# Kernel tuning notes

Hardware: AMD Instinct MI355X
Metric: run time of the kernel (lower is better)

Reference implementation:

```python
import jax, jax.numpy as jnp
import numpy as np

jax.config.update("jax_enable_x64", True)

NNZ = 8_388_608        # number of sparse (feature_id, value) pairs
N_FEATURES = 8_192     # number of calibrated feature ids
N_BIN = 63             # bin boundaries per feature -> 64 bins
OUT_BITS = 22          # output id space = 1 << 22
GOLDEN32 = np.uint32(0x9E3779B9)  # Knuth multiplicative-hashing constant


def setup_inputs() -> dict:
    key = jax.random.key(0)
    k1, k2, k3 = jax.random.split(key, 3)
    input_keys = jax.random.randint(k1, (NNZ,), 0, 2 * N_FEATURES, dtype=jnp.int64)
    input_vals = jax.random.normal(k2, (NNZ,), dtype=jnp.float32)
    # Calibrated feature ids (sorted) and per-feature sorted bin boundaries.
    feature_ids = jnp.arange(N_FEATURES, dtype=jnp.int64)
    bin_vals = jnp.sort(
        jax.random.normal(k3, (N_FEATURES, N_BIN), dtype=jnp.float32), axis=1
    ).reshape(-1)
    return {
        "input_keys": input_keys,
        "input_vals": input_vals,
        "feature_ids": feature_ids,
        "bin_vals": bin_vals,
    }


def _lower_bound_bins(bin_vals_flat, feat_idx, vals, n_bin):
    """Per-value branchless binary search: bin = sum(bin_row < val).

    bin_vals_flat: [F * n_bin] row-sorted boundaries, feat_idx: [nnz] int,
    vals: [nnz] float. Returns [nnz] int32 bin index in [0, n_bin].
    """
    steps = int(np.ceil(np.log2(n_bin + 1)))  # 6 for n_bin=63
    base = feat_idx.astype(jnp.int64) * n_bin
    lo = jnp.zeros(vals.shape, dtype=jnp.int32)
    hi = jnp.full(vals.shape, n_bin, dtype=jnp.int32)
    for _ in range(steps):
        mid = (lo + hi) >> 1                       # in [0, n_bin]
        mid_safe = jnp.minimum(mid, n_bin - 1)     # gather-safe
        bv = bin_vals_flat[base + mid_safe]
        valid = lo < hi
        go_right = valid & (bv < vals)             # strict '<' => lower bound
        lo = jnp.where(go_right, mid + 1, lo)
        hi = jnp.where(valid & ~go_right, mid, hi)
    return lo


def reference(input_keys, input_vals, feature_ids, bin_vals):
    F = feature_ids.shape[0]
    n_bin = bin_vals.shape[0] // F
    mask = jnp.int64((1 << OUT_BITS) - 1)

    # --- find each key in the (sorted) calibrated feature-id table ---
    idx = jnp.searchsorted(feature_ids, input_keys)          # [nnz]
    idx_safe = jnp.minimum(idx, F - 1)
    calibrated = feature_ids[idx_safe] == input_keys          # [nnz] bool

    # --- bin assignment: bin = sum(bin_vals_row < val) ---
    bins = _lower_bound_bins(bin_vals, idx_safe, input_vals, n_bin)

    # --- 32-bit integer multiplicative hash of (feature_id, bin) ---
    h = (input_keys.astype(jnp.uint32) * GOLDEN32 + bins.astype(jnp.uint32)) * GOLDEN32
    hashed_key = h.astype(jnp.int64) & mask

    out_keys = jnp.where(calibrated, hashed_key, input_keys & mask)
    out_vals = jnp.where(calibrated, jnp.ones_like(input_vals), input_vals)
    # dense_shape of the resulting SparseTensor is [batch, 1 << OUT_BITS]
    return out_keys, out_vals
```

## Files before the change

### kernel.cpp

```cpp
#include <hip/hip_runtime.h>
#include <stdint.h>
#include <math.h>


#define GOLDEN   0x9E3779B9u
#define OUT_MASK ((1u << 22) - 1u)
#define NBIN  63
#define NPIV  8192
#define NKEY  16384
#define MAGIC 0xC0FFEE42u

typedef float fx4 __attribute__((ext_vector_type(4)));
typedef int   ix4 __attribute__((ext_vector_type(4)));
typedef unsigned ux4 __attribute__((ext_vector_type(4)));

__global__ __launch_bounds__(256) void build_tables_kernel(
    const int* __restrict__ fids, const float* __restrict__ bins,
    float* __restrict__ qtab, ux4* __restrict__ spiv_g,
    unsigned char* __restrict__ scal_g, int F)
{
    const int t = blockIdx.x * blockDim.x + threadIdx.x;
    if (t >= F * 64) return;
    const int r = t >> 6;
    const int j = t & 63;
    const int k = fids[r];
    const unsigned uk = (unsigned)k;
    const float* src = bins + (size_t)r * NBIN;

    if (uk < (unsigned)NPIV) {
        qtab[((size_t)uk << 6) + j] = (j < NBIN) ? src[j] : INFINITY;
        if (j == 0) {
            ux4 p;
            p.x = __float_as_uint(src[15]);
            p.y = __float_as_uint(src[31]);
            p.z = __float_as_uint(src[47]);
            p.w = uk ^ MAGIC;
            spiv_g[uk] = p;
        }
    } else if (uk < (unsigned)NKEY && j == 0) {
        scal_g[uk - NPIV] = (unsigned char)(0x40u | (uk & 63u));
    }
}

__device__ __forceinline__ void hd_fallback(
    int k, float v, const int* __restrict__ fids, const float* __restrict__ bins,
    int F, int fsteps, float& okey, float& oval)
{
    int lo = 0, hi = F;
    for (int s = 0; s < fsteps; ++s) {
        int  mid  = (lo + hi) >> 1;
        int  mids = min(mid, F - 1);
        int  fv   = fids[mids];
        bool valid = lo < hi;
        bool right = valid && (fv < k);
        lo = right ? mid + 1 : lo;
        hi = (valid && !right) ? mid : hi;
    }
    const int  idx_safe   = min(lo, F - 1);
    const bool calibrated = (fids[idx_safe] == k);
    const float* brow = bins + (size_t)idx_safe * NBIN;
    int blo = 0, bhi = NBIN;
    #pragma unroll
    for (int s = 0; s < 6; ++s) {
        int   mid  = (blo + bhi) >> 1;
        int   mids = min(mid, NBIN - 1);
        float bv   = brow[mids];
        bool  valid = blo < bhi;
        bool  right = valid && (bv < v);
        blo = right ? mid + 1 : blo;
        bhi = (valid && !right) ? mid : bhi;
    }
    const uint32_t h = ((uint32_t)k * GOLDEN + (uint32_t)blo) * GOLDEN;
    okey = calibrated ? (float)(h & OUT_MASK) : (float)((uint32_t)k & OUT_MASK);
    oval = calibrated ? 1.0f : v;
}

__device__ __forceinline__ int hd_cmp8(fx4 a, fx4 b, float v) {
    return (a.x < v) + (a.y < v) + (a.z < v) + (a.w < v)
         + (b.x < v) + (b.y < v) + (b.z < v) + (b.w < v);
}

__global__ __launch_bounds__(1024, 4) void hd_main_kernel(
    const int* __restrict__ keys, const float* __restrict__ vals,
    const int* __restrict__ fids, const float* __restrict__ bins,
    const float* __restrict__ qtab, const ux4* __restrict__ spiv_g,
    const unsigned char* __restrict__ scal_g,
    float* __restrict__ out_keys, float* __restrict__ out_vals,
    int n, int F, int fsteps, int nchunks)
{
    extern __shared__ char smem[];
    ux4*      spiv = reinterpret_cast<ux4*>(smem);
    unsigned* scal = reinterpret_cast<unsigned*>(smem + (size_t)NPIV * 16);

    const int tid = threadIdx.x;
    for (int i = tid; i < NPIV; i += (int)blockDim.x) spiv[i] = spiv_g[i];
    const unsigned* scal_g32 = reinterpret_cast<const unsigned*>(scal_g);
    for (int i = tid; i < NPIV / 4; i += (int)blockDim.x) scal[i] = scal_g32[i];
    __syncthreads();

    const unsigned char* scal_b = reinterpret_cast<const unsigned char*>(scal);
    const char* qb = reinterpret_cast<const char*>(qtab);
    const int nthreads = (int)(gridDim.x * blockDim.x);

    for (int c = blockIdx.x * blockDim.x + tid; c < nchunks; c += nthreads) {
        const int i0 = c * 4;
        int   k0, k1, k2, k3;
        float v0, v1, v2, v3;
        const bool full = (i0 + 3 < n);
        if (full) {
            const ix4 ka = __builtin_nontemporal_load(reinterpret_cast<const ix4*>(keys + i0));
            const fx4 va = __builtin_nontemporal_load(reinterpret_cast<const fx4*>(vals + i0));
            k0 = ka.x; k1 = ka.y; k2 = ka.z; k3 = ka.w;
            v0 = va.x; v1 = va.y; v2 = va.z; v3 = va.w;
        } else {
            k0 = keys[min(i0 + 0, n - 1)]; v0 = vals[min(i0 + 0, n - 1)];
            k1 = keys[min(i0 + 1, n - 1)]; v1 = vals[min(i0 + 1, n - 1)];
            k2 = keys[min(i0 + 2, n - 1)]; v2 = vals[min(i0 + 2, n - 1)];
            k3 = keys[min(i0 + 3, n - 1)]; v3 = vals[min(i0 + 3, n - 1)];
        }

        const unsigned u0 = (unsigned)k0, u1 = (unsigned)k1,
                       u2 = (unsigned)k2, u3 = (unsigned)k3;
        const ux4 h0 = spiv[u0 < (unsigned)NPIV ? u0 : 0u];
        const ux4 h1 = spiv[u1 < (unsigned)NPIV ? u1 : 0u];
        const ux4 h2 = spiv[u2 < (unsigned)NPIV ? u2 : 0u];
        const ux4 h3 = spiv[u3 < (unsigned)NPIV ? u3 : 0u];

#define HD_P2(J)                                                              \
        const bool cal##J = (u##J < (unsigned)NPIV) &&                        \
                            (h##J.w == (u##J ^ MAGIC));                       \
        const int  q##J = (__uint_as_float(h##J.x) < v##J)                    \
                        + (__uint_as_float(h##J.y) < v##J)                    \
                        + (__uint_as_float(h##J.z) < v##J);                   \
        const unsigned off##J = cal##J ? ((u##J << 8) + (unsigned)(q##J << 6))\
                                       : 0u;                                  \
        int qc##J = q##J << 4;                                                \
        const unsigned hs##J = u##J - (unsigned)NPIV;                         \
        const bool rare##J =                                                  \
            (u##J >= (unsigned)NKEY) ||                                       \
            ((hs##J < (unsigned)NPIV) &&                                      \
             (scal_b[hs##J < (unsigned)NPIV ? hs##J : 0u] ==                  \
              (unsigned char)(0x40u | (u##J & 63u))));
        HD_P2(0) HD_P2(1) HD_P2(2) HD_P2(3)
#undef HD_P2

        fx4 a0 = *reinterpret_cast<const fx4*>(qb + off0);
        fx4 b0 = *reinterpret_cast<const fx4*>(qb + off0 + 16);
        fx4 a1 = *reinterpret_cast<const fx4*>(qb + off1);
        fx4 b1 = *reinterpret_cast<const fx4*>(qb + off1 + 16);
        fx4 a2 = *reinterpret_cast<const fx4*>(qb + off2);
        fx4 b2 = *reinterpret_cast<const fx4*>(qb + off2 + 16);
        fx4 a3 = *reinterpret_cast<const fx4*>(qb + off3);
        fx4 b3 = *reinterpret_cast<const fx4*>(qb + off3 + 16);

        qc0 += hd_cmp8(a0, b0, v0);
        qc1 += hd_cmp8(a1, b1, v1);
        qc2 += hd_cmp8(a2, b2, v2);
        qc3 += hd_cmp8(a3, b3, v3);

        a0 = *reinterpret_cast<const fx4*>(qb + off0 + 32);
        b0 = *reinterpret_cast<const fx4*>(qb + off0 + 48);
        a1 = *reinterpret_cast<const fx4*>(qb + off1 + 32);
        b1 = *reinterpret_cast<const fx4*>(qb + off1 + 48);
        a2 = *reinterpret_cast<const fx4*>(qb + off2 + 32);
        b2 = *reinterpret_cast<const fx4*>(qb + off2 + 48);
        a3 = *reinterpret_cast<const fx4*>(qb + off3 + 32);
        b3 = *reinterpret_cast<const fx4*>(qb + off3 + 48);

        float ok0, ok1, ok2, ok3, ov0, ov1, ov2, ov3;
#define HD_P6(J)                                                              \
        {                                                                     \
            const int cnt = qc##J + hd_cmp8(a##J, b##J, v##J);                \
            const uint32_t h = (u##J * GOLDEN + (uint32_t)cnt) * GOLDEN;      \
            ok##J = cal##J ? (float)(h & OUT_MASK) : (float)(u##J & OUT_MASK);\
            ov##J = cal##J ? 1.0f : v##J;                                     \
        }
        HD_P6(0) HD_P6(1) HD_P6(2) HD_P6(3)
#undef HD_P6

        if (__builtin_expect(rare0 | rare1 | rare2 | rare3, 0)) {
            if (rare0) hd_fallback(k0, v0, fids, bins, F, fsteps, ok0, ov0);
            if (rare1) hd_fallback(k1, v1, fids, bins, F, fsteps, ok1, ov1);
            if (rare2) hd_fallback(k2, v2, fids, bins, F, fsteps, ok2, ov2);
            if (rare3) hd_fallback(k3, v3, fids, bins, F, fsteps, ok3, ov3);
        }

        if (full) {
            fx4 s;
            s.x = ok0; s.y = ok1; s.z = ok2; s.w = ok3;
            __builtin_nontemporal_store(s, reinterpret_cast<fx4*>(out_keys + i0));
            s.x = ov0; s.y = ov1; s.z = ov2; s.w = ov3;
            __builtin_nontemporal_store(s, reinterpret_cast<fx4*>(out_vals + i0));
        } else {
            if (i0 + 0 < n) { out_keys[i0 + 0] = ok0; out_vals[i0 + 0] = ov0; }
            if (i0 + 1 < n) { out_keys[i0 + 1] = ok1; out_vals[i0 + 1] = ov1; }
            if (i0 + 2 < n) { out_keys[i0 + 2] = ok2; out_vals[i0 + 2] = ov2; }
            if (i0 + 3 < n) { out_keys[i0 + 3] = ok3; out_vals[i0 + 3] = ov3; }
        }
    }
}

__global__ __launch_bounds__(256) void hd_simple_kernel(
    const int* __restrict__ keys, const float* __restrict__ vals,
    const int* __restrict__ fids, const float* __restrict__ bins,
    float* __restrict__ out_keys, float* __restrict__ out_vals,
    int n, int F, int fsteps)
{
    const int gid = blockIdx.x * blockDim.x + threadIdx.x;
    const int i0 = gid * 4;
    if (i0 >= n) return;
    #pragma unroll
    for (int j = 0; j < 4; ++j) {
        int idx = min(i0 + j, n - 1);
        float okey, oval;
        hd_fallback(keys[idx], vals[idx], fids, bins, F, fsteps, okey, oval);
        if (i0 + j < n) { out_keys[i0 + j] = okey; out_vals[i0 + j] = oval; }
    }
}

extern "C" void kernel_launch(void* const* d_in, const int* in_sizes, int n_in,
                              void* d_out, int out_size, void* d_ws, size_t ws_size,
                              hipStream_t stream) {
    const int*   keys = (const int*)d_in[0];
    const float* vals = (const float*)d_in[1];
    const int*   fids = (const int*)d_in[2];
    const float* bins = (const float*)d_in[3];

    const int n = in_sizes[0];
    const int F = in_sizes[2];

    int fsteps = 0;
    while ((1 << fsteps) < F + 1) ++fsteps;

    float* out_keys = (float*)d_out;
    float* out_vals = (float*)d_out + n;

    const size_t qtab_bytes = (size_t)NPIV * 64 * sizeof(float);
    const size_t spiv_bytes = (size_t)NPIV * 16;
    const size_t scal_bytes = (size_t)NPIV;
    const size_t ws_need    = qtab_bytes + spiv_bytes + scal_bytes;
    const size_t lds_bytes  = spiv_bytes + scal_bytes;

    int max_lds = 0;
    hipDeviceGetAttribute(&max_lds, hipDeviceAttributeMaxSharedMemoryPerBlock, 0);

    const bool fast = (ws_size >= ws_need) && ((size_t)max_lds >= lds_bytes) &&
                      (in_sizes[3] == F * NBIN);

    if (fast) {
        float*         qtab   = (float*)d_ws;
        ux4*           spiv_g = (ux4*)((char*)d_ws + qtab_bytes);
        unsigned char* scal_g = (unsigned char*)d_ws + qtab_bytes + spiv_bytes;

        build_tables_kernel<<<(F * 64 + 255) / 256, 256, 0, stream>>>(
            fids, bins, qtab, spiv_g, scal_g, F);

        (void)hipFuncSetAttribute(
            reinterpret_cast<const void*>(hd_main_kernel),
            hipFuncAttributeMaxDynamicSharedMemorySize, (int)lds_bytes);

        const int threads = 1024;
        const int nblocks = 256;
        const int nchunks = (n + 3) / 4;
        hd_main_kernel<<<nblocks, threads, lds_bytes, stream>>>(
            keys, vals, fids, bins, qtab, spiv_g, scal_g,
            out_keys, out_vals, n, F, fsteps, nchunks);
    } else {
        const int threads = 256;
        const int grid = (n + threads * 4 - 1) / (threads * 4);
        hd_simple_kernel<<<grid, threads, 0, stream>>>(
            keys, vals, fids, bins, out_keys, out_vals, n, F, fsteps);
    }
}
```

Measured before the change: 164.9 us.

## Replace LDS 4-way pivot table with global 8-way pivots and 8-wide leaf gathers

The first level of the bin search now uses 7 pivots per feature (every 8th boundary), stored as a 32-byte record in global memory, so the second level reads one 8-float group (two 16-byte loads) instead of four. The per-block LDS staging of the pivot and scal tables and its barrier are removed, and their lookups now go through the cache hierarchy. The launch changes from 256x1024 threads with large dynamic LDS to up to 2048 blocks of 256 threads. This cuts gather traffic per element and the LDS prologue, but it replaces fast LDS lookups with global loads, which relies on the 256KB pivot table staying cache-resident.

```diff
diff --git a/kernel.cpp b/kernel.cpp
--- a/kernel.cpp
+++ b/kernel.cpp
@@ -16,26 +16,35 @@
 
 __global__ __launch_bounds__(256) void build_tables_kernel(
     const int* __restrict__ fids, const float* __restrict__ bins,
-    float* __restrict__ qtab, ux4* __restrict__ spiv_g,
+    float* __restrict__ wtab, ux4* __restrict__ ftab,
     unsigned char* __restrict__ scal_g, int F)
 {
     const int t = blockIdx.x * blockDim.x + threadIdx.x;
     if (t >= F * 64) return;
     const int r = t >> 6;
     const int j = t & 63;
-    const int k = fids[r];
-    const unsigned uk = (unsigned)k;
+    const unsigned uk = (unsigned)fids[r];
     const float* src = bins + (size_t)r * NBIN;
 
     if (uk < (unsigned)NPIV) {
-        qtab[((size_t)uk << 6) + j] = (j < NBIN) ? src[j] : INFINITY;
+        const int w = j >> 3, s = j & 7;
+        float val;
+        if (s < 7)      val = src[8 * w + s];
+        else if (w < 7) val = src[8 * w + 7];
+        else            val = INFINITY;
+        wtab[((size_t)uk << 6) + j] = val;
         if (j == 0) {
-            ux4 p;
-            p.x = __float_as_uint(src[15]);
-            p.y = __float_as_uint(src[31]);
-            p.z = __float_as_uint(src[47]);
-            p.w = uk ^ MAGIC;
-            spiv_g[uk] = p;
+            ux4 p0, p1;
+            p0.x = __float_as_uint(src[7]);
+            p0.y = __float_as_uint(src[15]);
+            p0.z = __float_as_uint(src[23]);
+            p0.w = __float_as_uint(src[31]);
+            p1.x = __float_as_uint(src[39]);
+            p1.y = __float_as_uint(src[47]);
+            p1.z = __float_as_uint(src[55]);
+            p1.w = uk ^ MAGIC;
+            ftab[uk * 2]     = p0;
+            ftab[uk * 2 + 1] = p1;
         }
     } else if (uk < (unsigned)NKEY && j == 0) {
         scal_g[uk - NPIV] = (unsigned char)(0x40u | (uk & 63u));
@@ -80,29 +89,19 @@
          + (b.x < v) + (b.y < v) + (b.z < v) + (b.w < v);
 }
 
-__global__ __launch_bounds__(1024, 4) void hd_main_kernel(
+__global__ __launch_bounds__(256) void hd_main_kernel(
     const int* __restrict__ keys, const float* __restrict__ vals,
     const int* __restrict__ fids, const float* __restrict__ bins,
-    const float* __restrict__ qtab, const ux4* __restrict__ spiv_g,
+    const float* __restrict__ wtab, const ux4* __restrict__ ftab,
     const unsigned char* __restrict__ scal_g,
     float* __restrict__ out_keys, float* __restrict__ out_vals,
     int n, int F, int fsteps, int nchunks)
 {
-    extern __shared__ char smem[];
-    ux4*      spiv = reinterpret_cast<ux4*>(smem);
-    unsigned* scal = reinterpret_cast<unsigned*>(smem + (size_t)NPIV * 16);
-
-    const int tid = threadIdx.x;
-    for (int i = tid; i < NPIV; i += (int)blockDim.x) spiv[i] = spiv_g[i];
-    const unsigned* scal_g32 = reinterpret_cast<const unsigned*>(scal_g);
-    for (int i = tid; i < NPIV / 4; i += (int)blockDim.x) scal[i] = scal_g32[i];
-    __syncthreads();
-
-    const unsigned char* scal_b = reinterpret_cast<const unsigned char*>(scal);
-    const char* qb = reinterpret_cast<const char*>(qtab);
+    const char* wb = reinterpret_cast<const char*>(wtab);
     const int nthreads = (int)(gridDim.x * blockDim.x);
 
-    for (int c = blockIdx.x * blockDim.x + tid; c < nchunks; c += nthreads) {
+    for (int c = blockIdx.x * blockDim.x + threadIdx.x; c < nchunks;
+         c += nthreads) {
         const int i0 = c * 4;
         int   k0, k1, k2, k3;
         float v0, v1, v2, v3;
@@ -121,62 +120,55 @@
 
         const unsigned u0 = (unsigned)k0, u1 = (unsigned)k1,
                        u2 = (unsigned)k2, u3 = (unsigned)k3;
-        const ux4 h0 = spiv[u0 < (unsigned)NPIV ? u0 : 0u];
-        const ux4 h1 = spiv[u1 < (unsigned)NPIV ? u1 : 0u];
-        const ux4 h2 = spiv[u2 < (unsigned)NPIV ? u2 : 0u];
-        const ux4 h3 = spiv[u3 < (unsigned)NPIV ? u3 : 0u];
+
+#define HD_P1(J)                                                              \
+        const unsigned ia##J = (u##J < (unsigned)NPIV) ? u##J : 0u;           \
+        const ux4 fa##J = ftab[ia##J * 2];                                    \
+        const ux4 fb##J = ftab[ia##J * 2 + 1];                                \
+        const unsigned hs##J = u##J - (unsigned)NPIV;                         \
+        const unsigned char sb##J =                                           \
+            scal_g[hs##J < (unsigned)NPIV ? hs##J : 0u];
+        HD_P1(0) HD_P1(1) HD_P1(2) HD_P1(3)
+#undef HD_P1
 
 #define HD_P2(J)                                                              \
         const bool cal##J = (u##J < (unsigned)NPIV) &&                        \
-                            (h##J.w == (u##J ^ MAGIC));                       \
-        const int  q##J = (__uint_as_float(h##J.x) < v##J)                    \
-                        + (__uint_as_float(h##J.y) < v##J)                    \
-                        + (__uint_as_float(h##J.z) < v##J);                   \
-        const unsigned off##J = cal##J ? ((u##J << 8) + (unsigned)(q##J << 6))\
-                                       : 0u;                                  \
-        int qc##J = q##J << 4;                                                \
-        const unsigned hs##J = u##J - (unsigned)NPIV;                         \
+                            (fb##J.w == (u##J ^ MAGIC));                      \
+        const int c##J = (__uint_as_float(fa##J.x) < v##J)                    \
+                       + (__uint_as_float(fa##J.y) < v##J)                    \
+                       + (__uint_as_float(fa##J.z) < v##J)                    \
+                       + (__uint_as_float(fa##J.w) < v##J)                    \
+                       + (__uint_as_float(fb##J.x) < v##J)                    \
+                       + (__uint_as_float(fb##J.y) < v##J)                    \
+                       + (__uint_as_float(fb##J.z) < v##J);                   \
+        const unsigned off##J =                                               \
+            cal##J ? ((u##J << 8) + (unsigned)(c##J << 5)) : 0u;              \
         const bool rare##J =                                                  \
             (u##J >= (unsigned)NKEY) ||                                       \
             ((hs##J < (unsigned)NPIV) &&                                      \
-             (scal_b[hs##J < (unsigned)NPIV ? hs##J : 0u] ==                  \
-              (unsigned char)(0x40u | (u##J & 63u))));
+             (sb##J == (unsigned char)(0x40u | (u##J & 63u))));
         HD_P2(0) HD_P2(1) HD_P2(2) HD_P2(3)
 #undef HD_P2
 
-        fx4 a0 = *reinterpret_cast<const fx4*>(qb + off0);
-        fx4 b0 = *reinterpret_cast<const fx4*>(qb + off0 + 16);
-        fx4 a1 = *reinterpret_cast<const fx4*>(qb + off1);
-        fx4 b1 = *reinterpret_cast<const fx4*>(qb + off1 + 16);
-        fx4 a2 = *reinterpret_cast<const fx4*>(qb + off2);
-        fx4 b2 = *reinterpret_cast<const fx4*>(qb + off2 + 16);
-        fx4 a3 = *reinterpret_cast<const fx4*>(qb + off3);
-        fx4 b3 = *reinterpret_cast<const fx4*>(qb + off3 + 16);
-
-        qc0 += hd_cmp8(a0, b0, v0);
-        qc1 += hd_cmp8(a1, b1, v1);
-        qc2 += hd_cmp8(a2, b2, v2);
-        qc3 += hd_cmp8(a3, b3, v3);
-
-        a0 = *reinterpret_cast<const fx4*>(qb + off0 + 32);
-        b0 = *reinterpret_cast<const fx4*>(qb + off0 + 48);
-        a1 = *reinterpret_cast<const fx4*>(qb + off1 + 32);
-        b1 = *reinterpret_cast<const fx4*>(qb + off1 + 48);
-        a2 = *reinterpret_cast<const fx4*>(qb + off2 + 32);
-        b2 = *reinterpret_cast<const fx4*>(qb + off2 + 48);
-        a3 = *reinterpret_cast<const fx4*>(qb + off3 + 32);
-        b3 = *reinterpret_cast<const fx4*>(qb + off3 + 48);
+        const fx4 a0 = *reinterpret_cast<const fx4*>(wb + off0);
+        const fx4 b0 = *reinterpret_cast<const fx4*>(wb + off0 + 16);
+        const fx4 a1 = *reinterpret_cast<const fx4*>(wb + off1);
+        const fx4 b1 = *reinterpret_cast<const fx4*>(wb + off1 + 16);
+        const fx4 a2 = *reinterpret_cast<const fx4*>(wb + off2);
+        const fx4 b2 = *reinterpret_cast<const fx4*>(wb + off2 + 16);
+        const fx4 a3 = *reinterpret_cast<const fx4*>(wb + off3);
+        const fx4 b3 = *reinterpret_cast<const fx4*>(wb + off3 + 16);
 
         float ok0, ok1, ok2, ok3, ov0, ov1, ov2, ov3;
-#define HD_P6(J)                                                              \
+#define HD_P4(J)                                                              \
         {                                                                     \
-            const int cnt = qc##J + hd_cmp8(a##J, b##J, v##J);                \
+            const int cnt = (c##J << 3) + hd_cmp8(a##J, b##J, v##J);          \
             const uint32_t h = (u##J * GOLDEN + (uint32_t)cnt) * GOLDEN;      \
             ok##J = cal##J ? (float)(h & OUT_MASK) : (float)(u##J & OUT_MASK);\
             ov##J = cal##J ? 1.0f : v##J;                                     \
         }
-        HD_P6(0) HD_P6(1) HD_P6(2) HD_P6(3)
-#undef HD_P6
+        HD_P4(0) HD_P4(1) HD_P4(2) HD_P4(3)
+#undef HD_P4
 
         if (__builtin_expect(rare0 | rare1 | rare2 | rare3, 0)) {
             if (rare0) hd_fallback(k0, v0, fids, bins, F, fsteps, ok0, ov0);
@@ -235,35 +227,27 @@
     float* out_keys = (float*)d_out;
     float* out_vals = (float*)d_out + n;
 
-    const size_t qtab_bytes = (size_t)NPIV * 64 * sizeof(float);
-    const size_t spiv_bytes = (size_t)NPIV * 16;
+    const size_t wtab_bytes = (size_t)NPIV * 64 * sizeof(float);
+    const size_t ftab_bytes = (size_t)NPIV * 32;
     const size_t scal_bytes = (size_t)NPIV;
-    const size_t ws_need    = qtab_bytes + spiv_bytes + scal_bytes;
-    const size_t lds_bytes  = spiv_bytes + scal_bytes;
-
-    int max_lds = 0;
-    hipDeviceGetAttribute(&max_lds, hipDeviceAttributeMaxSharedMemoryPerBlock, 0);
-
-    const bool fast = (ws_size >= ws_need) && ((size_t)max_lds >= lds_bytes) &&
-                      (in_sizes[3] == F * NBIN);
+    const size_t ws_need    = wtab_bytes + ftab_bytes + scal_bytes;
+
+    const bool fast = (ws_size >= ws_need) && (in_sizes[3] == F * NBIN);
 
     if (fast) {
-        float*         qtab   = (float*)d_ws;
-        ux4*           spiv_g = (ux4*)((char*)d_ws + qtab_bytes);
-        unsigned char* scal_g = (unsigned char*)d_ws + qtab_bytes + spiv_bytes;
+        float*         wtab   = (float*)d_ws;
+        ux4*           ftab   = (ux4*)((char*)d_ws + wtab_bytes);
+        unsigned char* scal_g = (unsigned char*)d_ws + wtab_bytes + ftab_bytes;
 
         build_tables_kernel<<<(F * 64 + 255) / 256, 256, 0, stream>>>(
-            fids, bins, qtab, spiv_g, scal_g, F);
-
-        (void)hipFuncSetAttribute(
-            reinterpret_cast<const void*>(hd_main_kernel),
-            hipFuncAttributeMaxDynamicSharedMemorySize, (int)lds_bytes);
-
-        const int threads = 1024;
-        const int nblocks = 256;
+            fids, bins, wtab, ftab, scal_g, F);
+
+        const int threads = 256;
         const int nchunks = (n + 3) / 4;
-        hd_main_kernel<<<nblocks, threads, lds_bytes, stream>>>(
-            keys, vals, fids, bins, qtab, spiv_g, scal_g,
+        int nblocks = (nchunks + threads - 1) / threads;
+        if (nblocks > 2048) nblocks = 2048;
+        hd_main_kernel<<<nblocks, threads, 0, stream>>>(
+            keys, vals, fids, bins, wtab, ftab, scal_g,
             out_keys, out_vals, n, F, fsteps, nchunks);
     } else {
         const int threads = 256;
```

After: 174.7 us. +6.0%, slower.

## Compress LDS pivot table to packed bf16 and raise occupancy

Applied to the files above, without the earlier changes.

The per-feature pivot entry in LDS shrinks from 16 to 8 bytes by storing the three quartile pivots as rounded-up bf16 values plus a 16-bit tag. The quartile guess is then fixed up by a loop that advances to the next 16-bin quad when all sixteen compares succeed. Smaller LDS use and 8 blocks per CU in launch bounds, with 512 blocks in the grid, aim to raise occupancy for this gather-latency-bound kernel. Uncalibrated keys now skip the qtab gather through a branch. The costs are an occasional extra 64-byte gather and divergence from the per-lane branches and retry loop.

```diff
diff --git a/kernel.cpp b/kernel.cpp
--- a/kernel.cpp
+++ b/kernel.cpp
@@ -8,34 +8,40 @@
 #define NBIN  63
 #define NPIV  8192
 #define NKEY  16384
-#define MAGIC 0xC0FFEE42u
 
 typedef float fx4 __attribute__((ext_vector_type(4)));
 typedef int   ix4 __attribute__((ext_vector_type(4)));
-typedef unsigned ux4 __attribute__((ext_vector_type(4)));
+typedef unsigned ux2 __attribute__((ext_vector_type(2)));
+
+__device__ __forceinline__ unsigned bf16c(float x) {
+    const unsigned b = __float_as_uint(x);
+    unsigned t = ((int)b >= 0) ? ((b + 0xFFFFu) >> 16) : (b >> 16);
+    return (t == 0x8000u) ? 0u : t;
+}
 
 __global__ __launch_bounds__(256) void build_tables_kernel(
     const int* __restrict__ fids, const float* __restrict__ bins,
-    float* __restrict__ qtab, ux4* __restrict__ spiv_g,
+    float* __restrict__ qtab, ux2* __restrict__ spiv8_g,
     unsigned char* __restrict__ scal_g, int F)
 {
     const int t = blockIdx.x * blockDim.x + threadIdx.x;
     if (t >= F * 64) return;
     const int r = t >> 6;
     const int j = t & 63;
-    const int k = fids[r];
-    const unsigned uk = (unsigned)k;
+    const unsigned uk = (unsigned)fids[r];
     const float* src = bins + (size_t)r * NBIN;
 
     if (uk < (unsigned)NPIV) {
         qtab[((size_t)uk << 6) + j] = (j < NBIN) ? src[j] : INFINITY;
         if (j == 0) {
-            ux4 p;
-            p.x = __float_as_uint(src[15]);
-            p.y = __float_as_uint(src[31]);
-            p.z = __float_as_uint(src[47]);
-            p.w = uk ^ MAGIC;
-            spiv_g[uk] = p;
+            const unsigned B15 = bf16c(src[15]);
+            const unsigned B31 = bf16c(src[31]);
+            const unsigned B47 = bf16c(src[47]);
+            const unsigned tag = 0x6000u | uk;
+            ux2 p;
+            p.x = B15 | (B31 << 16);
+            p.y = B47 | (tag << 16);
+            spiv8_g[uk] = p;
         }
     } else if (uk < (unsigned)NKEY && j == 0) {
         scal_g[uk - NPIV] = (unsigned char)(0x40u | (uk & 63u));
@@ -80,20 +86,35 @@
          + (b.x < v) + (b.y < v) + (b.z < v) + (b.w < v);
 }
 
-__global__ __launch_bounds__(1024, 4) void hd_main_kernel(
+__device__ __forceinline__ int hd_quad_bin(const char* qb, unsigned u,
+                                           float v, int q)
+{
+    for (;;) {
+        const char* p = qb + ((u << 8) + (unsigned)(q << 6));
+        const fx4 a = *reinterpret_cast<const fx4*>(p);
+        const fx4 b = *reinterpret_cast<const fx4*>(p + 16);
+        const fx4 c = *reinterpret_cast<const fx4*>(p + 32);
+        const fx4 d = *reinterpret_cast<const fx4*>(p + 48);
+        const int cnt = hd_cmp8(a, b, v) + hd_cmp8(c, d, v);
+        if (__builtin_expect(cnt == 16 && q < 3, 0)) { ++q; continue; }
+        return (q << 4) + cnt;
+    }
+}
+
+__global__ __launch_bounds__(1024, 8) void hd_main_kernel(
     const int* __restrict__ keys, const float* __restrict__ vals,
     const int* __restrict__ fids, const float* __restrict__ bins,
-    const float* __restrict__ qtab, const ux4* __restrict__ spiv_g,
+    const float* __restrict__ qtab, const ux2* __restrict__ spiv8_g,
     const unsigned char* __restrict__ scal_g,
     float* __restrict__ out_keys, float* __restrict__ out_vals,
     int n, int F, int fsteps, int nchunks)
 {
     extern __shared__ char smem[];
-    ux4*      spiv = reinterpret_cast<ux4*>(smem);
-    unsigned* scal = reinterpret_cast<unsigned*>(smem + (size_t)NPIV * 16);
+    ux2*      spiv8 = reinterpret_cast<ux2*>(smem);
+    unsigned* scal  = reinterpret_cast<unsigned*>(smem + (size_t)NPIV * 8);
 
     const int tid = threadIdx.x;
-    for (int i = tid; i < NPIV; i += (int)blockDim.x) spiv[i] = spiv_g[i];
+    for (int i = tid; i < NPIV; i += (int)blockDim.x) spiv8[i] = spiv8_g[i];
     const unsigned* scal_g32 = reinterpret_cast<const unsigned*>(scal_g);
     for (int i = tid; i < NPIV / 4; i += (int)blockDim.x) scal[i] = scal_g32[i];
     __syncthreads();
@@ -121,20 +142,19 @@
 
         const unsigned u0 = (unsigned)k0, u1 = (unsigned)k1,
                        u2 = (unsigned)k2, u3 = (unsigned)k3;
-        const ux4 h0 = spiv[u0 < (unsigned)NPIV ? u0 : 0u];
-        const ux4 h1 = spiv[u1 < (unsigned)NPIV ? u1 : 0u];
-        const ux4 h2 = spiv[u2 < (unsigned)NPIV ? u2 : 0u];
-        const ux4 h3 = spiv[u3 < (unsigned)NPIV ? u3 : 0u];
-
+
+        const ux2 h0 = spiv8[u0 < (unsigned)NPIV ? u0 : 0u];
+        const ux2 h1 = spiv8[u1 < (unsigned)NPIV ? u1 : 0u];
+        const ux2 h2 = spiv8[u2 < (unsigned)NPIV ? u2 : 0u];
+        const ux2 h3 = spiv8[u3 < (unsigned)NPIV ? u3 : 0u];
+
+#define HD_BF(B) __uint_as_float((B) << 16)
 #define HD_P2(J)                                                              \
         const bool cal##J = (u##J < (unsigned)NPIV) &&                        \
-                            (h##J.w == (u##J ^ MAGIC));                       \
-        const int  q##J = (__uint_as_float(h##J.x) < v##J)                    \
-                        + (__uint_as_float(h##J.y) < v##J)                    \
-                        + (__uint_as_float(h##J.z) < v##J);                   \
-        const unsigned off##J = cal##J ? ((u##J << 8) + (unsigned)(q##J << 6))\
-                                       : 0u;                                  \
-        int qc##J = q##J << 4;                                                \
+                            ((h##J.y >> 16) == (0x6000u | u##J));             \
+        const int q##J = (HD_BF(h##J.x & 0xFFFFu) < v##J)                     \
+                       + (HD_BF(h##J.x >> 16)     < v##J)                     \
+                       + (HD_BF(h##J.y & 0xFFFFu) < v##J);                    \
         const unsigned hs##J = u##J - (unsigned)NPIV;                         \
         const bool rare##J =                                                  \
             (u##J >= (unsigned)NKEY) ||                                       \
@@ -143,40 +163,21 @@
               (unsigned char)(0x40u | (u##J & 63u))));
         HD_P2(0) HD_P2(1) HD_P2(2) HD_P2(3)
 #undef HD_P2
-
-        fx4 a0 = *reinterpret_cast<const fx4*>(qb + off0);
-        fx4 b0 = *reinterpret_cast<const fx4*>(qb + off0 + 16);
-        fx4 a1 = *reinterpret_cast<const fx4*>(qb + off1);
-        fx4 b1 = *reinterpret_cast<const fx4*>(qb + off1 + 16);
-        fx4 a2 = *reinterpret_cast<const fx4*>(qb + off2);
-        fx4 b2 = *reinterpret_cast<const fx4*>(qb + off2 + 16);
-        fx4 a3 = *reinterpret_cast<const fx4*>(qb + off3);
-        fx4 b3 = *reinterpret_cast<const fx4*>(qb + off3 + 16);
-
-        qc0 += hd_cmp8(a0, b0, v0);
-        qc1 += hd_cmp8(a1, b1, v1);
-        qc2 += hd_cmp8(a2, b2, v2);
-        qc3 += hd_cmp8(a3, b3, v3);
-
-        a0 = *reinterpret_cast<const fx4*>(qb + off0 + 32);
-        b0 = *reinterpret_cast<const fx4*>(qb + off0 + 48);
-        a1 = *reinterpret_cast<const fx4*>(qb + off1 + 32);
-        b1 = *reinterpret_cast<const fx4*>(qb + off1 + 48);
-        a2 = *reinterpret_cast<const fx4*>(qb + off2 + 32);
-        b2 = *reinterpret_cast<const fx4*>(qb + off2 + 48);
-        a3 = *reinterpret_cast<const fx4*>(qb + off3 + 32);
-        b3 = *reinterpret_cast<const fx4*>(qb + off3 + 48);
+#undef HD_BF
 
         float ok0, ok1, ok2, ok3, ov0, ov1, ov2, ov3;
-#define HD_P6(J)                                                              \
-        {                                                                     \
-            const int cnt = qc##J + hd_cmp8(a##J, b##J, v##J);                \
-            const uint32_t h = (u##J * GOLDEN + (uint32_t)cnt) * GOLDEN;      \
-            ok##J = cal##J ? (float)(h & OUT_MASK) : (float)(u##J & OUT_MASK);\
-            ov##J = cal##J ? 1.0f : v##J;                                     \
-        }
-        HD_P6(0) HD_P6(1) HD_P6(2) HD_P6(3)
-#undef HD_P6
+#define HD_P3(J)                                                              \
+        if (cal##J) {                                                         \
+            const int bin = hd_quad_bin(qb, u##J, v##J, q##J);                \
+            const uint32_t h = (u##J * GOLDEN + (uint32_t)bin) * GOLDEN;      \
+            ok##J = (float)(h & OUT_MASK);                                    \
+            ov##J = 1.0f;                                                     \
+        } else {                                                              \
+            ok##J = (float)(u##J & OUT_MASK);                                 \
+            ov##J = v##J;                                                     \
+        }
+        HD_P3(0) HD_P3(1) HD_P3(2) HD_P3(3)
+#undef HD_P3
 
         if (__builtin_expect(rare0 | rare1 | rare2 | rare3, 0)) {
             if (rare0) hd_fallback(k0, v0, fids, bins, F, fsteps, ok0, ov0);
@@ -236,7 +237,7 @@
     float* out_vals = (float*)d_out + n;
 
     const size_t qtab_bytes = (size_t)NPIV * 64 * sizeof(float);
-    const size_t spiv_bytes = (size_t)NPIV * 16;
+    const size_t spiv_bytes = (size_t)NPIV * 8;
     const size_t scal_bytes = (size_t)NPIV;
     const size_t ws_need    = qtab_bytes + spiv_bytes + scal_bytes;
     const size_t lds_bytes  = spiv_bytes + scal_bytes;
@@ -245,25 +246,25 @@
     hipDeviceGetAttribute(&max_lds, hipDeviceAttributeMaxSharedMemoryPerBlock, 0);
 
     const bool fast = (ws_size >= ws_need) && ((size_t)max_lds >= lds_bytes) &&
-                      (in_sizes[3] == F * NBIN);
+                      (in_sizes[3] == F * NBIN) && (F <= NPIV);
 
     if (fast) {
-        float*         qtab   = (float*)d_ws;
-        ux4*           spiv_g = (ux4*)((char*)d_ws + qtab_bytes);
-        unsigned char* scal_g = (unsigned char*)d_ws + qtab_bytes + spiv_bytes;
+        float*         qtab    = (float*)d_ws;
+        ux2*           spiv8_g = (ux2*)((char*)d_ws + qtab_bytes);
+        unsigned char* scal_g  = (unsigned char*)d_ws + qtab_bytes + spiv_bytes;
 
         build_tables_kernel<<<(F * 64 + 255) / 256, 256, 0, stream>>>(
-            fids, bins, qtab, spiv_g, scal_g, F);
+            fids, bins, qtab, spiv8_g, scal_g, F);
 
         (void)hipFuncSetAttribute(
             reinterpret_cast<const void*>(hd_main_kernel),
             hipFuncAttributeMaxDynamicSharedMemorySize, (int)lds_bytes);
 
         const int threads = 1024;
-        const int nblocks = 256;
+        const int nblocks = 512;
         const int nchunks = (n + 3) / 4;
         hd_main_kernel<<<nblocks, threads, lds_bytes, stream>>>(
-            keys, vals, fids, bins, qtab, spiv_g, scal_g,
+            keys, vals, fids, bins, qtab, spiv8_g, scal_g,
             out_keys, out_vals, n, F, fsteps, nchunks);
     } else {
         const int threads = 256;
```

Result: faster. 159.8 us (-3.1%).
